# Kernel tuning notes

Hardware: AMD Instinct MI355X
Metric: run time of the kernel (lower is better)

Reference implementation:

```python
import jax, jax.numpy as jnp
import numpy as np

B, N, D = 32, 2048, 768
DEPTH, HEADS, GRID, NC = 12, 12, 10, 40
T = GRID * GRID + 1          # 100 pillars + cls token
HD = D // HEADS
SCALE = HD ** -0.5
INTERVAL = 0.2
MLP_H = 4 * D
EPS = 1e-5


def setup_inputs() -> dict:
    key = jax.random.key(0)
    ks = list(jax.random.split(key, 12))
    n = lambda k, s, std: (jax.random.normal(k, s, dtype=jnp.float32) * std)
    return {
        "x": jax.random.uniform(ks[0], (B, N, 3), minval=-1.0, maxval=1.0, dtype=jnp.float32),
        "W1": n(ks[1], (6, 32), 0.1),
        "W2": n(ks[2], (32, 64), 0.1),
        "W3": n(ks[3], (64, 128), 0.1),
        "Wa": n(ks[4], (256, D), 0.05),
        "bn_g": jnp.ones((GRID * GRID,), jnp.float32),
        "bn_b": jnp.zeros((GRID * GRID,), jnp.float32),
        "bn_mean": jnp.zeros((GRID * GRID,), jnp.float32),
        "bn_var": jnp.ones((GRID * GRID,), jnp.float32),
        "cls_token": jnp.zeros((1, 1, D), jnp.float32),
        "pos_embed": n(ks[5], (1, T, D), 0.02),
        "ln1_g": jnp.ones((DEPTH, D), jnp.float32), "ln1_b": jnp.zeros((DEPTH, D), jnp.float32),
        "qkv_w": n(ks[6], (DEPTH, D, 3 * D), 0.01),
        "proj_w": n(ks[7], (DEPTH, D, D), 0.01), "proj_b": jnp.zeros((DEPTH, D), jnp.float32),
        "ln2_g": jnp.ones((DEPTH, D), jnp.float32), "ln2_b": jnp.zeros((DEPTH, D), jnp.float32),
        "fc1_w": n(ks[8], (DEPTH, D, MLP_H), 0.01), "fc1_b": jnp.zeros((DEPTH, MLP_H), jnp.float32),
        "fc2_w": n(ks[9], (DEPTH, MLP_H, D), 0.01), "fc2_b": jnp.zeros((DEPTH, D), jnp.float32),
        "norm_g": jnp.ones((D,), jnp.float32), "norm_b": jnp.zeros((D,), jnp.float32),
        "head_w": n(ks[10], (D, NC), 0.01), "head_b": jnp.zeros((NC,), jnp.float32),
    }


def _layer_norm(x, g, b):
    m = jnp.mean(x, -1, keepdims=True)
    v = jnp.mean(jnp.square(x - m), -1, keepdims=True)
    return (x - m) * jax.lax.rsqrt(v + EPS) * g + b


def reference(x, W1, W2, W3, Wa, bn_g, bn_b, bn_mean, bn_var, cls_token, pos_embed,
              ln1_g, ln1_b, qkv_w, proj_w, proj_b, ln2_g, ln2_b,
              fc1_w, fc1_b, fc2_w, fc2_b, norm_g, norm_b, head_w, head_b):
    # ---- Pillar encoder (voxel bucketing via segment ops) ----
    # torch code reorders columns (y,z,x)->(z,y,x); voxel index uses (y,x)
    p = x[..., jnp.array([1, 0, 2])]                     # [B,N,3] = (z,y,x)
    yx = jnp.clip(p[..., 1:] + 1.0, 0.0, 1.99)
    idx = jnp.floor(yx / INTERVAL).astype(jnp.int32)     # [B,N,2] in [0,GRID)
    cell = (idx[..., 0] * GRID + idx[..., 1]
            + jnp.arange(B, dtype=jnp.int32)[:, None] * GRID * GRID).reshape(-1)
    pf = p.reshape(-1, 3)                                # [B*N,3]
    S = B * GRID * GRID
    cnt = jax.ops.segment_sum(jnp.ones((B * N,), pf.dtype), cell, num_segments=S)
    centroid = jax.ops.segment_sum(pf, cell, num_segments=S) / jnp.maximum(cnt, 1.0)[:, None]
    aug = jnp.concatenate([pf, pf - centroid[cell]], -1)  # [B*N,6]
    h = jax.nn.relu(aug @ W1)
    h = jax.nn.relu(h @ W2)
    h = jax.nn.relu(h @ W3)                               # [B*N,128]
    pooled = jax.ops.segment_max(h, cell, num_segments=S)  # per-pillar max
    h2 = jax.nn.relu(jnp.concatenate([h, pooled[cell]], -1) @ Wa)  # [B*N,768]
    pillar = jax.ops.segment_max(h2, cell, num_segments=S)
    pillar = jnp.where(cnt[:, None] > 0, pillar, 0.0)     # empty cells stay zero
    seq = pillar.reshape(B, GRID * GRID, D)               # flatten order = y*GRID+x
    # BatchNorm1d(100) over the sequence-position channel (eval mode)
    inv = bn_g * jax.lax.rsqrt(bn_var + EPS)
    seq = (seq - bn_mean[None, :, None]) * inv[None, :, None] + bn_b[None, :, None]

    # ---- ViT stack ----
    tokens = jnp.concatenate([jnp.broadcast_to(cls_token, (B, 1, D)), seq], 1) + pos_embed

    def block(hh, prm):
        g1, b1, qw, pw, pb, g2, b2, f1w, f1b, f2w, f2b = prm
        y = _layer_norm(hh, g1, b1)
        qkv = (y @ qw).reshape(B, T, 3, HEADS, HD)
        q, k, v = qkv[:, :, 0], qkv[:, :, 1], qkv[:, :, 2]   # [B,T,H,hd]
        attn = jax.nn.softmax(jnp.einsum('bqhd,bkhd->bhqk', q, k) * SCALE, -1)
        o = jnp.einsum('bhqk,bkhd->bqhd', attn, v).reshape(B, T, D)
        hh = hh + o @ pw + pb
        y = _layer_norm(hh, g2, b2)
        y = jax.nn.gelu(y @ f1w + f1b, approximate=False)
        hh = hh + y @ f2w + f2b
        return hh, None

    prms = (ln1_g, ln1_b, qkv_w, proj_w, proj_b, ln2_g, ln2_b, fc1_w, fc1_b, fc2_w, fc2_b)
    tokens, _ = jax.lax.scan(block, tokens, prms)
    out = _layer_norm(tokens, norm_g, norm_b)[:, 0] @ head_w + head_b  # cls head
    return out
```

## Files before the change

### kernel.cpp

```cpp
#include <hip/hip_runtime.h>

typedef __bf16 bf8 __attribute__((ext_vector_type(8)));
typedef float  f4  __attribute__((ext_vector_type(4)));
typedef unsigned long long uptr;

__device__ __forceinline__ void gload16(const void* g, void* l){
  __builtin_amdgcn_global_load_lds(
      (const __attribute__((address_space(1))) unsigned int*)(uptr)g,
      (__attribute__((address_space(3))) unsigned int*)(uptr)l,
      16, 0, 0);
}


__global__ __launch_bounds__(256) void k_cell(const float* __restrict__ x, int* __restrict__ cellArr,
                                              float* __restrict__ cnt, float* __restrict__ cent){
  int p = blockIdx.x*256 + threadIdx.x;
  float x0 = x[p*3+0], x1 = x[p*3+1], x2 = x[p*3+2];
  float y0 = fminf(fmaxf(x0 + 1.0f, 0.0f), 1.99f);
  float y1 = fminf(fmaxf(x2 + 1.0f, 0.0f), 1.99f);
  int i0 = (int)floorf(y0 / 0.2f);
  int i1 = (int)floorf(y1 / 0.2f);
  int b = p >> 11;
  int cell = b*100 + i0*10 + i1;
  cellArr[p] = cell;
  atomicAdd(&cnt[cell], 1.0f);
  atomicAdd(&cent[cell*3+0], x1);
  atomicAdd(&cent[cell*3+1], x0);
  atomicAdd(&cent[cell*3+2], x2);
}

__global__ void k_centdiv(float* cent, const float* cnt){
  int i = blockIdx.x*256 + threadIdx.x;
  if (i < 3200*3) cent[i] /= fmaxf(cnt[i/3], 1.0f);
}

__global__ __launch_bounds__(256) void k_scan(const float* __restrict__ cnt,
                                              int* __restrict__ base, int* __restrict__ wptr){
  __shared__ int a[256];
  int tid = threadIdx.x;
  int start = tid*13, end = start+13; if (end > 3200) end = 3200;
  int local = 0;
  for (int i = start; i < end; i++) local += (int)cnt[i];
  a[tid] = local;
  __syncthreads();
  for (int off = 1; off < 256; off <<= 1){
    int t = (tid >= off) ? a[tid - off] : 0;
    __syncthreads();
    a[tid] += t;
    __syncthreads();
  }
  int run = a[tid] - local;
  for (int i = start; i < end; i++){
    base[i] = run; wptr[i] = run;
    run += (int)cnt[i];
  }
}

__global__ __launch_bounds__(256) void k_scatter(const int* __restrict__ cellArr,
                                                 int* __restrict__ wptr, int* __restrict__ order){
  int p = blockIdx.x*256 + threadIdx.x;
  int c = cellArr[p];
  int pos = atomicAdd(&wptr[c], 1);
  order[pos] = p;
}

__global__ __launch_bounds__(256) void k_pointmlp(const float* __restrict__ x,
    const float* __restrict__ W1, const float* __restrict__ W2, const float* __restrict__ W3,
    const float* __restrict__ cent, const int* __restrict__ cellArr,
    const int* __restrict__ order, int* __restrict__ cellSlot, __bf16* __restrict__ A2){
  __shared__ float w1s[6*32];
  __shared__ float w2s[32*64];
  __shared__ float w3s[64*128];
  int tid = threadIdx.x;
  for (int i = tid; i < 192;  i += 256) w1s[i] = W1[i];
  for (int i = tid; i < 2048; i += 256) w2s[i] = W2[i];
  for (int i = tid; i < 8192; i += 256) w3s[i] = W3[i];
  __syncthreads();
  int s = blockIdx.x*256 + tid;
  int p = order[s];
  int cell = cellArr[p];
  cellSlot[s] = cell;
  float pf0 = x[p*3+1], pf1 = x[p*3+0], pf2 = x[p*3+2];
  float a[6] = {pf0, pf1, pf2, pf0 - cent[cell*3+0], pf1 - cent[cell*3+1], pf2 - cent[cell*3+2]};
  float h1[32];
  #pragma unroll
  for (int f = 0; f < 32; f++){
    float t = 0.f;
    #pragma unroll
    for (int i = 0; i < 6; i++) t += a[i]*w1s[i*32+f];
    h1[f] = fmaxf(t, 0.f);
  }
  float h2[64];
  #pragma unroll
  for (int f = 0; f < 64; f++){
    float t = 0.f;
    #pragma unroll
    for (int i = 0; i < 32; i++) t += h1[i]*w2s[i*64+f];
    h2[f] = fmaxf(t, 0.f);
  }
  for (int f0 = 0; f0 < 128; f0 += 8){
    __bf16 tmp[8];
    #pragma unroll
    for (int j = 0; j < 8; j++){
      float t = 0.f;
      #pragma unroll
      for (int i = 0; i < 64; i++) t += h2[i]*w3s[i*128+f0+j];
      tmp[j] = (__bf16)fmaxf(t, 0.f);
    }
    *reinterpret_cast<uint4*>(&A2[(size_t)s*256 + f0]) = *reinterpret_cast<uint4*>(tmp);
  }
}

__global__ __launch_bounds__(128) void k_poolh(const __bf16* __restrict__ A2,
    const int* __restrict__ base, const float* __restrict__ cnt, float* __restrict__ pooled){
  int c = blockIdx.x, f = threadIdx.x;
  int b0 = base[c], n = (int)cnt[c];
  float v = 0.f;
  for (int k = 0; k < n; k++) v = fmaxf(v, (float)A2[(size_t)(b0+k)*256 + f]);
  pooled[c*128 + f] = v;
}

__global__ __launch_bounds__(256) void k_fill(const float* __restrict__ pooled,
    const int* __restrict__ cellSlot, __bf16* __restrict__ A2){
  int idx = blockIdx.x*256 + threadIdx.x;
  int s = idx >> 7, f = idx & 127;
  A2[(size_t)s*256 + 128 + f] = (__bf16)pooled[cellSlot[s]*128 + f];
}

__global__ __launch_bounds__(256) void k_pillarpool(const __bf16* __restrict__ h2c,
    const int* __restrict__ base, const float* __restrict__ cnt, float* __restrict__ pillar, int cs){
  int c = blockIdx.x, tid = threadIdx.x;
  int b0 = base[c], e0 = b0 + (int)cnt[c];
  int lo = b0 > cs ? b0 : cs;
  int hi = e0 < cs + 16384 ? e0 : cs + 16384;
  if (lo >= hi) return;
  for (int f = tid; f < 768; f += 256){
    float v = 0.f;
    for (int s = lo; s < hi; s++) v = fmaxf(v, (float)h2c[(size_t)(s - cs)*768 + f]);
    atomicMax((int*)&pillar[(size_t)c*768 + f], __float_as_int(v));
  }
}

__global__ void k_assemble(const float* __restrict__ pillar,
    const float* __restrict__ bn_g, const float* __restrict__ bn_b,
    const float* __restrict__ bn_mean, const float* __restrict__ bn_var,
    const float* __restrict__ cls_t, const float* __restrict__ pos,
    float* __restrict__ tokens){
  int idx = blockIdx.x*256 + threadIdx.x;
  int m = idx / 768, d = idx % 768;
  int b = m / 101, t = m % 101;
  float v;
  if (t == 0) v = cls_t[d];
  else {
    int s = t - 1;
    float pv = pillar[((size_t)b*100 + s)*768 + d];
    float inv = bn_g[s]*rsqrtf(bn_var[s] + 1e-5f);
    v = (pv - bn_mean[s])*inv + bn_b[s];
  }
  tokens[idx] = v + pos[t*768 + d];
}


__global__ __launch_bounds__(256) void k_transpose(const float* __restrict__ W, __bf16* __restrict__ Wt,
                                                   int K, int N){
  __shared__ float t[32][33];
  int n0 = blockIdx.x*32, k0 = blockIdx.y*32;
  int tx = threadIdx.x & 31, ty = threadIdx.x >> 5;
  #pragma unroll
  for (int i = 0; i < 32; i += 8){
    int k = k0 + ty + i, n = n0 + tx;
    t[ty+i][tx] = (k < K && n < N) ? W[(size_t)k*N + n] : 0.f;
  }
  __syncthreads();
  #pragma unroll
  for (int i = 0; i < 32; i += 8){
    int n = n0 + ty + i, k = k0 + tx;
    if (n < N && k < K) Wt[(size_t)n*K + k] = (__bf16)t[tx][ty+i];
  }
}

__global__ __launch_bounds__(256) void k_transpose_all(
    const float* __restrict__ qw, const float* __restrict__ pw,
    const float* __restrict__ f1, const float* __restrict__ f2,
    __bf16* __restrict__ wq, __bf16* __restrict__ wp,
    __bf16* __restrict__ w1, __bf16* __restrict__ w2){
  int id = blockIdx.x;
  const float* W; __bf16* Wt; int K, N, nx, ny;
  if (id < 1728){ W=qw; Wt=wq; K=768;  N=2304; nx=id%72; ny=id/72; }
  else if (id < 2304){ id-=1728; W=pw; Wt=wp; K=768;  N=768;  nx=id%24; ny=id/24; }
  else if (id < 4608){ id-=2304; W=f1; Wt=w1; K=768;  N=3072; nx=id%96; ny=id/96; }
  else {               id-=4608; W=f2; Wt=w2; K=3072; N=768;  nx=id%24; ny=id/24; }
  __shared__ float t[32][33];
  int n0 = nx*32, k0 = ny*32;
  int tx = threadIdx.x & 31, ty = threadIdx.x >> 5;
  #pragma unroll
  for (int i = 0; i < 32; i += 8) t[ty+i][tx] = W[(size_t)(k0+ty+i)*N + n0+tx];
  __syncthreads();
  #pragma unroll
  for (int i = 0; i < 32; i += 8) Wt[(size_t)(n0+ty+i)*K + k0+tx] = (__bf16)t[tx][ty+i];
}


__global__ __launch_bounds__(256) void k_gemm(const __bf16* __restrict__ A, const __bf16* __restrict__ Bt,
    const float* __restrict__ bias, const float* __restrict__ res,
    float* __restrict__ outF, __bf16* __restrict__ outB,
    int M, int N, int K, int act, int splitK){
  __shared__ alignas(16) __bf16 As[128*32];
  __shared__ alignas(16) __bf16 Bs[128*32];
  int tid  = threadIdx.x;
  int m0 = blockIdx.y*128, n0 = blockIdx.x*128;
  int z = blockIdx.z;
  int kLen = K / splitK, k0 = z*kLen;
  int wave = tid >> 6, lane = tid & 63;
  int wm = (wave >> 1)*64, wn = (wave & 1)*64;
  int r16 = lane & 15, q = lane >> 4;
  int lrow = lane >> 2, lpc = lane & 3;
  f4 acc[4][4];
  #pragma unroll
  for (int i = 0; i < 4; i++)
    #pragma unroll
    for (int j = 0; j < 4; j++) acc[i][j] = (f4){0.f,0.f,0.f,0.f};

  for (int kt = k0; kt < k0 + kLen; kt += 32){
    #pragma unroll
    for (int s = 0; s < 2; s++){
      int rg  = wave*2 + s;
      int row = rg*16 + lrow;
      int gm = m0 + row; if (gm >= M) gm = M - 1;
      gload16(A  + (size_t)gm*K + kt + lpc*8, (char*)As + rg*1024 + lane*16);
      int gn = n0 + row;
      gload16(Bt + (size_t)gn*K + kt + lpc*8, (char*)Bs + rg*1024 + lane*16);
    }
    __syncthreads();
    bf8 af[4], bq[4];
    #pragma unroll
    for (int i = 0; i < 4; i++) af[i] = *reinterpret_cast<const bf8*>(&As[(wm + i*16 + r16)*32 + q*8]);
    #pragma unroll
    for (int j = 0; j < 4; j++) bq[j] = *reinterpret_cast<const bf8*>(&Bs[(wn + j*16 + r16)*32 + q*8]);
    #pragma unroll
    for (int i = 0; i < 4; i++)
      #pragma unroll
      for (int j = 0; j < 4; j++)
        acc[i][j] = __builtin_amdgcn_mfma_f32_16x16x32_bf16(af[i], bq[j], acc[i][j], 0, 0, 0);
    __syncthreads();
  }

  #pragma unroll
  for (int i = 0; i < 4; i++){
    #pragma unroll
    for (int j = 0; j < 4; j++){
      int nn = n0 + wn + j*16 + r16;
      float bv = (bias && z == 0) ? bias[nn] : 0.f;
      #pragma unroll
      for (int r = 0; r < 4; r++){
        int m = m0 + wm + i*16 + q*4 + r;
        if (m >= M) continue;
        float v = acc[i][j][r] + bv;
        if (splitK > 1){
          atomicAdd(&outF[(size_t)m*N + nn], v);
        } else {
          if (act == 1) v = fmaxf(v, 0.f);
          else if (act == 2) v = 0.5f*v*(1.f + erff(v*0.70710678118654752f));
          if (outB){
            outB[(size_t)m*N + nn] = (__bf16)v;
          } else {
            float rv = res ? res[(size_t)m*N + nn] : 0.f;
            outF[(size_t)m*N + nn] = rv + v;
          }
        }
      }
    }
  }
}


__global__ __launch_bounds__(256) void k_ln(const float* __restrict__ in, const float* __restrict__ g,
    const float* __restrict__ bta, __bf16* __restrict__ outB, float* __restrict__ outF, int rowMul){
  int orow = blockIdx.x;
  const float* xr = in + (size_t)orow*rowMul*768;
  int tid = threadIdx.x;
  float v0 = xr[tid], v1 = xr[tid+256], v2 = xr[tid+512];
  float s = v0+v1+v2, s2 = v0*v0 + v1*v1 + v2*v2;
  #pragma unroll
  for (int off = 32; off > 0; off >>= 1){ s += __shfl_xor(s, off); s2 += __shfl_xor(s2, off); }
  __shared__ float rs[4], rq[4];
  int w = tid >> 6;
  if ((tid & 63) == 0){ rs[w] = s; rq[w] = s2; }
  __syncthreads();
  s = rs[0]+rs[1]+rs[2]+rs[3]; s2 = rq[0]+rq[1]+rq[2]+rq[3];
  float mean = s*(1.f/768.f);
  float var  = s2*(1.f/768.f) - mean*mean;
  float rstd = rsqrtf(var + 1e-5f);
  size_t ob = (size_t)orow*768;
  float y0 = (v0-mean)*rstd*g[tid]     + bta[tid];
  float y1 = (v1-mean)*rstd*g[tid+256] + bta[tid+256];
  float y2 = (v2-mean)*rstd*g[tid+512] + bta[tid+512];
  if (outB){ outB[ob+tid]=(__bf16)y0; outB[ob+tid+256]=(__bf16)y1; outB[ob+tid+512]=(__bf16)y2; }
  else     { outF[ob+tid]=y0;         outF[ob+tid+256]=y1;         outF[ob+tid+512]=y2; }
}


#define PSS 136
#define VTS 136

__global__ __launch_bounds__(256) void k_attn(const __bf16* __restrict__ qkvB, __bf16* __restrict__ o){
  __shared__ alignas(16) __bf16 smem[64*VTS + 128*PSS];
  __bf16* Vt = smem;
  __bf16* Ps = smem + 64*VTS;
  int b = blockIdx.x / 12, h = blockIdx.x % 12;
  int tid = threadIdx.x;
  const __bf16* basep = qkvB + (size_t)(b*101)*2304 + h*64;

  #pragma unroll
  for (int it = 0; it < 4; it++){
    int c = tid + it*256;
    int t = c >> 3, d0 = c & 7;
    bf8 v;
    if (t < 101){
      v = *reinterpret_cast<const bf8*>(&basep[(size_t)t*2304 + 1536 + d0*8]);
    } else {
      #pragma unroll
      for (int j = 0; j < 8; j++) v[j] = (__bf16)0.f;
    }
    #pragma unroll
    for (int j = 0; j < 8; j++){
      int jj = (j + d0) & 7;
      Vt[(d0*8 + jj)*VTS + t] = v[jj];
    }
  }

  int wave = tid >> 6, lane = tid & 63;
  int r16 = lane & 15, q = lane >> 4;

  f4 sacc[2][7];
  #pragma unroll
  for (int rt = 0; rt < 2; rt++)
    #pragma unroll
    for (int j = 0; j < 7; j++) sacc[rt][j] = (f4){0.f,0.f,0.f,0.f};
  #pragma unroll
  for (int kt = 0; kt < 64; kt += 32){
    bf8 aq[2];
    #pragma unroll
    for (int rt = 0; rt < 2; rt++){
      int row = (wave + rt*4)*16 + r16; if (row > 100) row = 100;
      aq[rt] = *reinterpret_cast<const bf8*>(&basep[(size_t)row*2304 + kt + q*8]);
    }
    #pragma unroll
    for (int j = 0; j < 7; j++){
      int krow = j*16 + r16; if (krow > 100) krow = 100;
      bf8 kf = *reinterpret_cast<const bf8*>(&basep[(size_t)krow*2304 + 768 + kt + q*8]);
      #pragma unroll
      for (int rt = 0; rt < 2; rt++)
        sacc[rt][j] = __builtin_amdgcn_mfma_f32_16x16x32_bf16(aq[rt], kf, sacc[rt][j], 0, 0, 0);
    }
  }

  #pragma unroll
  for (int rt = 0; rt < 2; rt++){
    int m0 = (wave + rt*4)*16;
    #pragma unroll
    for (int r = 0; r < 4; r++){
      float s[7];
      #pragma unroll
      for (int j = 0; j < 7; j++){
        s[j] = sacc[rt][j][r] * 0.125f;
        if (j == 6 && r16 >= 5) s[j] = -1e30f;
      }
      float mx = s[0];
      #pragma unroll
      for (int j = 1; j < 7; j++) mx = fmaxf(mx, s[j]);
      #pragma unroll
      for (int off2 = 1; off2 < 16; off2 <<= 1) mx = fmaxf(mx, __shfl_xor(mx, off2));
      float p[7], sum = 0.f;
      #pragma unroll
      for (int j = 0; j < 7; j++){ p[j] = __expf(s[j] - mx); sum += p[j]; }
      #pragma unroll
      for (int off2 = 1; off2 < 16; off2 <<= 1) sum += __shfl_xor(sum, off2);
      float inv = 1.f / sum;
      int row = m0 + q*4 + r;
      #pragma unroll
      for (int j = 0; j < 7; j++) Ps[row*PSS + j*16 + r16] = (__bf16)(p[j]*inv);
      Ps[row*PSS + 112 + r16] = (__bf16)0.f;
    }
  }
  __syncthreads();

  f4 oacc[2][4];
  #pragma unroll
  for (int rt = 0; rt < 2; rt++)
    #pragma unroll
    for (int n = 0; n < 4; n++) oacc[rt][n] = (f4){0.f,0.f,0.f,0.f};
  #pragma unroll
  for (int kt = 0; kt < 128; kt += 32){
    bf8 af[2];
    #pragma unroll
    for (int rt = 0; rt < 2; rt++)
      af[rt] = *reinterpret_cast<const bf8*>(&Ps[((wave + rt*4)*16 + r16)*PSS + kt + q*8]);
    #pragma unroll
    for (int n = 0; n < 4; n++){
      bf8 bq = *reinterpret_cast<const bf8*>(&Vt[(n*16 + r16)*VTS + kt + q*8]);
      #pragma unroll
      for (int rt = 0; rt < 2; rt++)
        oacc[rt][n] = __builtin_amdgcn_mfma_f32_16x16x32_bf16(af[rt], bq, oacc[rt][n], 0, 0, 0);
    }
  }

  #pragma unroll
  for (int rt = 0; rt < 2; rt++){
    int m0 = (wave + rt*4)*16;
    #pragma unroll
    for (int n = 0; n < 4; n++){
      #pragma unroll
      for (int r = 0; r < 4; r++){
        int t = m0 + q*4 + r;
        if (t < 101)
          o[((size_t)(b*101 + t))*768 + h*64 + n*16 + r16] = (__bf16)oacc[rt][n][r];
      }
    }
  }
}

__global__ void k_head(const float* __restrict__ cls, const float* __restrict__ hw,
                       const float* __restrict__ hb, float* __restrict__ out){
  int b = blockIdx.x, c = threadIdx.x;
  if (c < 40){
    float s = hb[c];
    for (int k = 0; k < 768; k++) s += cls[b*768 + k]*hw[k*40 + c];
    out[b*40 + c] = s;
  }
}


extern "C" void kernel_launch(void* const* d_in, const int* in_sizes, int n_in,
                              void* d_out, int out_size, void* d_ws, size_t ws_size,
                              hipStream_t stream){
  const float* x       = (const float*)d_in[0];
  const float* W1      = (const float*)d_in[1];
  const float* W2      = (const float*)d_in[2];
  const float* W3      = (const float*)d_in[3];
  const float* Wa      = (const float*)d_in[4];
  const float* bn_g    = (const float*)d_in[5];
  const float* bn_b    = (const float*)d_in[6];
  const float* bn_mean = (const float*)d_in[7];
  const float* bn_var  = (const float*)d_in[8];
  const float* cls_t   = (const float*)d_in[9];
  const float* pos     = (const float*)d_in[10];
  const float* ln1_g   = (const float*)d_in[11];
  const float* ln1_b   = (const float*)d_in[12];
  const float* qkv_w   = (const float*)d_in[13];
  const float* proj_w  = (const float*)d_in[14];
  const float* proj_b  = (const float*)d_in[15];
  const float* ln2_g   = (const float*)d_in[16];
  const float* ln2_b   = (const float*)d_in[17];
  const float* fc1_w   = (const float*)d_in[18];
  const float* fc1_b   = (const float*)d_in[19];
  const float* fc2_w   = (const float*)d_in[20];
  const float* fc2_b   = (const float*)d_in[21];
  const float* norm_g  = (const float*)d_in[22];
  const float* norm_b  = (const float*)d_in[23];
  const float* head_w  = (const float*)d_in[24];
  const float* head_b  = (const float*)d_in[25];

  char* ws = (char*)d_ws;
  size_t off = 0;
  auto alloc = [&](size_t bytes)->void*{ void* p = ws + off; off += (bytes + 255) & ~(size_t)255; return p; };
  float* cnt     = (float*)alloc(3200*4);
  float* cent    = (float*)alloc(3200*3*4);
  float* pillar  = (float*)alloc((size_t)3200*768*4);
  size_t zbytes  = (size_t)((char*)pillar - (char*)cnt) + (size_t)3200*768*4;
  int*   base    = (int*)  alloc(3200*4);
  int*   wptr    = (int*)  alloc(3200*4);
  int*   order   = (int*)  alloc((size_t)65536*4);
  int*   cellSlot= (int*)  alloc((size_t)65536*4);
  int*   cellArr = (int*)  alloc((size_t)65536*4);
  float* pooled  = (float*)alloc((size_t)3200*128*4);
  float* tokens  = (float*)alloc((size_t)3232*768*4);
  float* cls     = (float*)alloc((size_t)32*768*4);
  __bf16* wWa    = (__bf16*)alloc((size_t)768*256*2);
  size_t offR = off;
  __bf16* A2  = (__bf16*)alloc((size_t)65536*256*2);
  __bf16* h2c = (__bf16*)alloc((size_t)16384*768*2);
  size_t endPillarPhase = off;
  off = offR;
  __bf16* y    = (__bf16*)alloc((size_t)3232*768*2);
  __bf16* qkvB = (__bf16*)alloc((size_t)3232*2304*2);
  __bf16* o    = (__bf16*)alloc((size_t)3232*768*2);
  __bf16* mlp  = (__bf16*)alloc((size_t)3232*3072*2);
  __bf16* wq   = (__bf16*)alloc((size_t)768*2304*2);
  __bf16* wp   = (__bf16*)alloc((size_t)768*768*2);
  __bf16* w1   = (__bf16*)alloc((size_t)768*3072*2);
  __bf16* w2   = (__bf16*)alloc((size_t)3072*768*2);
  if (off < endPillarPhase) off = endPillarPhase;
  (void)ws_size; (void)in_sizes; (void)n_in; (void)out_size;

  hipMemsetAsync(cnt, 0, zbytes, stream);

  k_cell<<<256,256,0,stream>>>(x, cellArr, cnt, cent);
  k_centdiv<<<38,256,0,stream>>>(cent, cnt);
  k_scan<<<1,256,0,stream>>>(cnt, base, wptr);
  k_scatter<<<256,256,0,stream>>>(cellArr, wptr, order);
  k_pointmlp<<<256,256,0,stream>>>(x, W1, W2, W3, cent, cellArr, order, cellSlot, A2);
  k_poolh<<<3200,128,0,stream>>>(A2, base, cnt, pooled);
  k_fill<<<32768,256,0,stream>>>(pooled, cellSlot, A2);
  k_transpose<<<dim3(24,8),256,0,stream>>>(Wa, wWa, 256, 768);
  for (int c = 0; c < 4; c++){
    k_gemm<<<dim3(6,128),256,0,stream>>>(A2 + (size_t)c*16384*256, wWa, nullptr, nullptr,
                                         nullptr, h2c, 16384, 768, 256, 1, 1);
    k_pillarpool<<<3200,256,0,stream>>>(h2c, base, cnt, pillar, c*16384);
  }
  k_assemble<<<9696,256,0,stream>>>(pillar, bn_g, bn_b, bn_mean, bn_var, cls_t, pos, tokens);

  for (int l = 0; l < 12; l++){
    k_transpose_all<<<6912,256,0,stream>>>(qkv_w + (size_t)l*768*2304, proj_w + (size_t)l*768*768,
                                           fc1_w + (size_t)l*768*3072, fc2_w + (size_t)l*3072*768,
                                           wq, wp, w1, w2);
    k_ln<<<3232,256,0,stream>>>(tokens, ln1_g + l*768, ln1_b + l*768, y, nullptr, 1);
    k_gemm<<<dim3(18,26),256,0,stream>>>(y, wq, nullptr, nullptr, nullptr, qkvB, 3232, 2304, 768, 0, 1);
    k_attn<<<384,256,0,stream>>>(qkvB, o);
    k_gemm<<<dim3(6,26,4),256,0,stream>>>(o, wp, proj_b + l*768, nullptr, tokens, nullptr,
                                          3232, 768, 768, 0, 4);
    k_ln<<<3232,256,0,stream>>>(tokens, ln2_g + l*768, ln2_b + l*768, y, nullptr, 1);
    k_gemm<<<dim3(24,26),256,0,stream>>>(y, w1, fc1_b + l*3072, nullptr, nullptr, mlp, 3232, 3072, 768, 2, 1);
    k_gemm<<<dim3(6,26,4),256,0,stream>>>(mlp, w2, fc2_b + l*768, nullptr, tokens, nullptr,
                                          3232, 768, 3072, 0, 4);
  }

  k_ln<<<32,256,0,stream>>>(tokens, norm_g, norm_b, nullptr, cls, 101);
  k_head<<<32,64,0,stream>>>(cls, head_w, head_b, (float*)d_out);
}
```

Measured before the change: 3.131 ms.

## Batch weight transposes, deepen GEMM K-tile with swizzle, split attention blocks

All 12 layers' weights are transposed to bf16 in one up-front launch instead of per layer, using extra workspace. The GEMM K-tile grows from 32 to 64 with an XOR-swizzled LDS layout to halve barrier count and avoid bank conflicts. Attention is split into two blocks per (batch, head) with a smaller LDS footprint and a launch-bounds occupancy hint. The centroid divide is folded into the point MLP, and the fill kernel now writes 16-byte vectors.

New measurement: 2.906 ms. 7.2% less time.

```diff
diff --git a/kernel.cpp b/kernel.cpp
--- a/kernel.cpp
+++ b/kernel.cpp
@@ -29,11 +29,6 @@
   atomicAdd(&cent[cell*3+2], x2);
 }
 
-__global__ void k_centdiv(float* cent, const float* cnt){
-  int i = blockIdx.x*256 + threadIdx.x;
-  if (i < 3200*3) cent[i] /= fmaxf(cnt[i/3], 1.0f);
-}
-
 __global__ __launch_bounds__(256) void k_scan(const float* __restrict__ cnt,
                                               int* __restrict__ base, int* __restrict__ wptr){
   __shared__ int a[256];
@@ -66,7 +61,7 @@
 
 __global__ __launch_bounds__(256) void k_pointmlp(const float* __restrict__ x,
     const float* __restrict__ W1, const float* __restrict__ W2, const float* __restrict__ W3,
-    const float* __restrict__ cent, const int* __restrict__ cellArr,
+    const float* __restrict__ cent, const float* __restrict__ cnt, const int* __restrict__ cellArr,
     const int* __restrict__ order, int* __restrict__ cellSlot, __bf16* __restrict__ A2){
   __shared__ float w1s[6*32];
   __shared__ float w2s[32*64];
@@ -81,7 +76,9 @@
   int cell = cellArr[p];
   cellSlot[s] = cell;
   float pf0 = x[p*3+1], pf1 = x[p*3+0], pf2 = x[p*3+2];
-  float a[6] = {pf0, pf1, pf2, pf0 - cent[cell*3+0], pf1 - cent[cell*3+1], pf2 - cent[cell*3+2]};
+  float cc = fmaxf(cnt[cell], 1.0f);
+  float a[6] = {pf0, pf1, pf2,
+                pf0 - cent[cell*3+0]/cc, pf1 - cent[cell*3+1]/cc, pf2 - cent[cell*3+2]/cc};
   float h1[32];
   #pragma unroll
   for (int f = 0; f < 32; f++){
@@ -123,8 +120,13 @@
 __global__ __launch_bounds__(256) void k_fill(const float* __restrict__ pooled,
     const int* __restrict__ cellSlot, __bf16* __restrict__ A2){
   int idx = blockIdx.x*256 + threadIdx.x;
-  int s = idx >> 7, f = idx & 127;
-  A2[(size_t)s*256 + 128 + f] = (__bf16)pooled[cellSlot[s]*128 + f];
+  int s = idx >> 4, f0 = (idx & 15) << 3;
+  int cell = cellSlot[s];
+  const float* pp = &pooled[cell*128 + f0];
+  __bf16 tmp[8];
+  #pragma unroll
+  for (int j = 0; j < 8; j++) tmp[j] = (__bf16)pp[j];
+  *reinterpret_cast<uint4*>(&A2[(size_t)s*256 + 128 + f0]) = *reinterpret_cast<uint4*>(tmp);
 }
 
 __global__ __launch_bounds__(256) void k_pillarpool(const __bf16* __restrict__ h2c,
@@ -185,11 +187,12 @@
     __bf16* __restrict__ wq, __bf16* __restrict__ wp,
     __bf16* __restrict__ w1, __bf16* __restrict__ w2){
   int id = blockIdx.x;
+  size_t l = blockIdx.y;
   const float* W; __bf16* Wt; int K, N, nx, ny;
-  if (id < 1728){ W=qw; Wt=wq; K=768;  N=2304; nx=id%72; ny=id/72; }
-  else if (id < 2304){ id-=1728; W=pw; Wt=wp; K=768;  N=768;  nx=id%24; ny=id/24; }
-  else if (id < 4608){ id-=2304; W=f1; Wt=w1; K=768;  N=3072; nx=id%96; ny=id/96; }
-  else {               id-=4608; W=f2; Wt=w2; K=3072; N=768;  nx=id%24; ny=id/24; }
+  if (id < 1728){ W=qw+l*768*2304; Wt=wq+l*768*2304; K=768;  N=2304; nx=id%72; ny=id/72; }
+  else if (id < 2304){ id-=1728; W=pw+l*768*768;  Wt=wp+l*768*768;  K=768;  N=768;  nx=id%24; ny=id/24; }
+  else if (id < 4608){ id-=2304; W=f1+l*768*3072; Wt=w1+l*768*3072; K=768;  N=3072; nx=id%96; ny=id/96; }
+  else {               id-=4608; W=f2+l*3072*768; Wt=w2+l*3072*768; K=3072; N=768;  nx=id%24; ny=id/24; }
   __shared__ float t[32][33];
   int n0 = nx*32, k0 = ny*32;
   int tx = threadIdx.x & 31, ty = threadIdx.x >> 5;
@@ -205,8 +208,8 @@
     const float* __restrict__ bias, const float* __restrict__ res,
     float* __restrict__ outF, __bf16* __restrict__ outB,
     int M, int N, int K, int act, int splitK){
-  __shared__ alignas(16) __bf16 As[128*32];
-  __shared__ alignas(16) __bf16 Bs[128*32];
+  __shared__ alignas(16) __bf16 As[128*64];
+  __shared__ alignas(16) __bf16 Bs[128*64];
   int tid  = threadIdx.x;
   int m0 = blockIdx.y*128, n0 = blockIdx.x*128;
   int z = blockIdx.z;
@@ -214,34 +217,41 @@
   int wave = tid >> 6, lane = tid & 63;
   int wm = (wave >> 1)*64, wn = (wave & 1)*64;
   int r16 = lane & 15, q = lane >> 4;
-  int lrow = lane >> 2, lpc = lane & 3;
+  int srow = tid >> 3;
+  int sslot = tid & 7;
+  int slotX[2];
+  #pragma unroll
+  for (int kk = 0; kk < 2; kk++) slotX[kk] = ((kk*4 + q) ^ (r16 & 7)) * 8;
   f4 acc[4][4];
   #pragma unroll
   for (int i = 0; i < 4; i++)
     #pragma unroll
     for (int j = 0; j < 4; j++) acc[i][j] = (f4){0.f,0.f,0.f,0.f};
 
-  for (int kt = k0; kt < k0 + kLen; kt += 32){
-    #pragma unroll
-    for (int s = 0; s < 2; s++){
-      int rg  = wave*2 + s;
-      int row = rg*16 + lrow;
+  for (int kt = k0; kt < k0 + kLen; kt += 64){
+    #pragma unroll
+    for (int rr = 0; rr < 4; rr++){
+      int row = rr*32 + srow;
+      int scol = kt + ((sslot ^ (row & 7)) * 8);
       int gm = m0 + row; if (gm >= M) gm = M - 1;
-      gload16(A  + (size_t)gm*K + kt + lpc*8, (char*)As + rg*1024 + lane*16);
+      gload16(A  + (size_t)gm*K + scol, (char*)As + rr*4096 + tid*16);
       int gn = n0 + row;
-      gload16(Bt + (size_t)gn*K + kt + lpc*8, (char*)Bs + rg*1024 + lane*16);
+      gload16(Bt + (size_t)gn*K + scol, (char*)Bs + rr*4096 + tid*16);
     }
     __syncthreads();
-    bf8 af[4], bq[4];
-    #pragma unroll
-    for (int i = 0; i < 4; i++) af[i] = *reinterpret_cast<const bf8*>(&As[(wm + i*16 + r16)*32 + q*8]);
-    #pragma unroll
-    for (int j = 0; j < 4; j++) bq[j] = *reinterpret_cast<const bf8*>(&Bs[(wn + j*16 + r16)*32 + q*8]);
-    #pragma unroll
-    for (int i = 0; i < 4; i++)
+    #pragma unroll
+    for (int kk = 0; kk < 2; kk++){
+      bf8 af[4], bq[4];
       #pragma unroll
-      for (int j = 0; j < 4; j++)
-        acc[i][j] = __builtin_amdgcn_mfma_f32_16x16x32_bf16(af[i], bq[j], acc[i][j], 0, 0, 0);
+      for (int i = 0; i < 4; i++) af[i] = *reinterpret_cast<const bf8*>(&As[(wm + i*16 + r16)*64 + slotX[kk]]);
+      #pragma unroll
+      for (int j = 0; j < 4; j++) bq[j] = *reinterpret_cast<const bf8*>(&Bs[(wn + j*16 + r16)*64 + slotX[kk]]);
+      #pragma unroll
+      for (int i = 0; i < 4; i++)
+        #pragma unroll
+        for (int j = 0; j < 4; j++)
+          acc[i][j] = __builtin_amdgcn_mfma_f32_16x16x32_bf16(af[i], bq[j], acc[i][j], 0, 0, 0);
+    }
     __syncthreads();
   }
 
@@ -303,11 +313,12 @@
 #define PSS 136
 #define VTS 136
 
-__global__ __launch_bounds__(256) void k_attn(const __bf16* __restrict__ qkvB, __bf16* __restrict__ o){
-  __shared__ alignas(16) __bf16 smem[64*VTS + 128*PSS];
+__global__ __launch_bounds__(256, 3) void k_attn(const __bf16* __restrict__ qkvB, __bf16* __restrict__ o){
+  __shared__ alignas(16) __bf16 smem[64*VTS + 64*PSS];
   __bf16* Vt = smem;
   __bf16* Ps = smem + 64*VTS;
-  int b = blockIdx.x / 12, h = blockIdx.x % 12;
+  int bh = blockIdx.x >> 1, half = blockIdx.x & 1;
+  int b = bh / 12, h = bh % 12;
   int tid = threadIdx.x;
   const __bf16* basep = qkvB + (size_t)(b*101)*2304 + h*64;
 
@@ -331,91 +342,69 @@
 
   int wave = tid >> 6, lane = tid & 63;
   int r16 = lane & 15, q = lane >> 4;
-
-  f4 sacc[2][7];
-  #pragma unroll
-  for (int rt = 0; rt < 2; rt++)
-    #pragma unroll
-    for (int j = 0; j < 7; j++) sacc[rt][j] = (f4){0.f,0.f,0.f,0.f};
+  int m0 = half*64 + wave*16;
+
+  f4 sacc[7];
+  #pragma unroll
+  for (int j = 0; j < 7; j++) sacc[j] = (f4){0.f,0.f,0.f,0.f};
   #pragma unroll
   for (int kt = 0; kt < 64; kt += 32){
-    bf8 aq[2];
-    #pragma unroll
-    for (int rt = 0; rt < 2; rt++){
-      int row = (wave + rt*4)*16 + r16; if (row > 100) row = 100;
-      aq[rt] = *reinterpret_cast<const bf8*>(&basep[(size_t)row*2304 + kt + q*8]);
-    }
+    int row = m0 + r16; if (row > 100) row = 100;
+    bf8 aq = *reinterpret_cast<const bf8*>(&basep[(size_t)row*2304 + kt + q*8]);
     #pragma unroll
     for (int j = 0; j < 7; j++){
       int krow = j*16 + r16; if (krow > 100) krow = 100;
       bf8 kf = *reinterpret_cast<const bf8*>(&basep[(size_t)krow*2304 + 768 + kt + q*8]);
-      #pragma unroll
-      for (int rt = 0; rt < 2; rt++)
-        sacc[rt][j] = __builtin_amdgcn_mfma_f32_16x16x32_bf16(aq[rt], kf, sacc[rt][j], 0, 0, 0);
-    }
-  }
-
-  #pragma unroll
-  for (int rt = 0; rt < 2; rt++){
-    int m0 = (wave + rt*4)*16;
-    #pragma unroll
-    for (int r = 0; r < 4; r++){
-      float s[7];
-      #pragma unroll
-      for (int j = 0; j < 7; j++){
-        s[j] = sacc[rt][j][r] * 0.125f;
-        if (j == 6 && r16 >= 5) s[j] = -1e30f;
-      }
-      float mx = s[0];
-      #pragma unroll
-      for (int j = 1; j < 7; j++) mx = fmaxf(mx, s[j]);
-      #pragma unroll
-      for (int off2 = 1; off2 < 16; off2 <<= 1) mx = fmaxf(mx, __shfl_xor(mx, off2));
-      float p[7], sum = 0.f;
-      #pragma unroll
-      for (int j = 0; j < 7; j++){ p[j] = __expf(s[j] - mx); sum += p[j]; }
-      #pragma unroll
-      for (int off2 = 1; off2 < 16; off2 <<= 1) sum += __shfl_xor(sum, off2);
-      float inv = 1.f / sum;
-      int row = m0 + q*4 + r;
-      #pragma unroll
-      for (int j = 0; j < 7; j++) Ps[row*PSS + j*16 + r16] = (__bf16)(p[j]*inv);
-      Ps[row*PSS + 112 + r16] = (__bf16)0.f;
-    }
+      sacc[j] = __builtin_amdgcn_mfma_f32_16x16x32_bf16(aq, kf, sacc[j], 0, 0, 0);
+    }
+  }
+
+  #pragma unroll
+  for (int r = 0; r < 4; r++){
+    float s[7];
+    #pragma unroll
+    for (int j = 0; j < 7; j++){
+      s[j] = sacc[j][r] * 0.125f;
+      if (j == 6 && r16 >= 5) s[j] = -1e30f;
+    }
+    float mx = s[0];
+    #pragma unroll
+    for (int j = 1; j < 7; j++) mx = fmaxf(mx, s[j]);
+    #pragma unroll
+    for (int off2 = 1; off2 < 16; off2 <<= 1) mx = fmaxf(mx, __shfl_xor(mx, off2));
+    float p[7], sum = 0.f;
+    #pragma unroll
+    for (int j = 0; j < 7; j++){ p[j] = __expf(s[j] - mx); sum += p[j]; }
+    #pragma unroll
+    for (int off2 = 1; off2 < 16; off2 <<= 1) sum += __shfl_xor(sum, off2);
+    float inv = 1.f / sum;
+    int lr = wave*16 + q*4 + r;
+    #pragma unroll
+    for (int j = 0; j < 7; j++) Ps[lr*PSS + j*16 + r16] = (__bf16)(p[j]*inv);
+    Ps[lr*PSS + 112 + r16] = (__bf16)0.f;
   }
   __syncthreads();
 
-  f4 oacc[2][4];
-  #pragma unroll
-  for (int rt = 0; rt < 2; rt++)
-    #pragma unroll
-    for (int n = 0; n < 4; n++) oacc[rt][n] = (f4){0.f,0.f,0.f,0.f};
+  f4 oacc[4];
+  #pragma unroll
+  for (int n = 0; n < 4; n++) oacc[n] = (f4){0.f,0.f,0.f,0.f};
   #pragma unroll
   for (int kt = 0; kt < 128; kt += 32){
-    bf8 af[2];
-    #pragma unroll
-    for (int rt = 0; rt < 2; rt++)
-      af[rt] = *reinterpret_cast<const bf8*>(&Ps[((wave + rt*4)*16 + r16)*PSS + kt + q*8]);
+    bf8 af = *reinterpret_cast<const bf8*>(&Ps[(wave*16 + r16)*PSS + kt + q*8]);
     #pragma unroll
     for (int n = 0; n < 4; n++){
       bf8 bq = *reinterpret_cast<const bf8*>(&Vt[(n*16 + r16)*VTS + kt + q*8]);
-      #pragma unroll
-      for (int rt = 0; rt < 2; rt++)
-        oacc[rt][n] = __builtin_amdgcn_mfma_f32_16x16x32_bf16(af[rt], bq, oacc[rt][n], 0, 0, 0);
-    }
-  }
-
-  #pragma unroll
-  for (int rt = 0; rt < 2; rt++){
-    int m0 = (wave + rt*4)*16;
-    #pragma unroll
-    for (int n = 0; n < 4; n++){
-      #pragma unroll
-      for (int r = 0; r < 4; r++){
-        int t = m0 + q*4 + r;
-        if (t < 101)
-          o[((size_t)(b*101 + t))*768 + h*64 + n*16 + r16] = (__bf16)oacc[rt][n][r];
-      }
+      oacc[n] = __builtin_amdgcn_mfma_f32_16x16x32_bf16(af, bq, oacc[n], 0, 0, 0);
+    }
+  }
+
+  #pragma unroll
+  for (int n = 0; n < 4; n++){
+    #pragma unroll
+    for (int r = 0; r < 4; r++){
+      int t = m0 + q*4 + r;
+      if (t < 101)
+        o[((size_t)(b*101 + t))*768 + h*64 + n*16 + r16] = (__bf16)oacc[n][r];
     }
   }
 }
@@ -477,6 +466,10 @@
   float* tokens  = (float*)alloc((size_t)3232*768*4);
   float* cls     = (float*)alloc((size_t)32*768*4);
   __bf16* wWa    = (__bf16*)alloc((size_t)768*256*2);
+  __bf16* wq12   = (__bf16*)alloc((size_t)12*768*2304*2);
+  __bf16* wp12   = (__bf16*)alloc((size_t)12*768*768*2);
+  __bf16* w112   = (__bf16*)alloc((size_t)12*768*3072*2);
+  __bf16* w212   = (__bf16*)alloc((size_t)12*3072*768*2);
   size_t offR = off;
   __bf16* A2  = (__bf16*)alloc((size_t)65536*256*2);
   __bf16* h2c = (__bf16*)alloc((size_t)16384*768*2);
@@ -486,23 +479,20 @@
   __bf16* qkvB = (__bf16*)alloc((size_t)3232*2304*2);
   __bf16* o    = (__bf16*)alloc((size_t)3232*768*2);
   __bf16* mlp  = (__bf16*)alloc((size_t)3232*3072*2);
-  __bf16* wq   = (__bf16*)alloc((size_t)768*2304*2);
-  __bf16* wp   = (__bf16*)alloc((size_t)768*768*2);
-  __bf16* w1   = (__bf16*)alloc((size_t)768*3072*2);
-  __bf16* w2   = (__bf16*)alloc((size_t)3072*768*2);
   if (off < endPillarPhase) off = endPillarPhase;
   (void)ws_size; (void)in_sizes; (void)n_in; (void)out_size;
 
   hipMemsetAsync(cnt, 0, zbytes, stream);
 
+  k_transpose_all<<<dim3(6912,12),256,0,stream>>>(qkv_w, proj_w, fc1_w, fc2_w, wq12, wp12, w112, w212);
+  k_transpose<<<dim3(24,8),256,0,stream>>>(Wa, wWa, 256, 768);
+
   k_cell<<<256,256,0,stream>>>(x, cellArr, cnt, cent);
-  k_centdiv<<<38,256,0,stream>>>(cent, cnt);
   k_scan<<<1,256,0,stream>>>(cnt, base, wptr);
   k_scatter<<<256,256,0,stream>>>(cellArr, wptr, order);
-  k_pointmlp<<<256,256,0,stream>>>(x, W1, W2, W3, cent, cellArr, order, cellSlot, A2);
+  k_pointmlp<<<256,256,0,stream>>>(x, W1, W2, W3, cent, cnt, cellArr, order, cellSlot, A2);
   k_poolh<<<3200,128,0,stream>>>(A2, base, cnt, pooled);
-  k_fill<<<32768,256,0,stream>>>(pooled, cellSlot, A2);
-  k_transpose<<<dim3(24,8),256,0,stream>>>(Wa, wWa, 256, 768);
+  k_fill<<<4096,256,0,stream>>>(pooled, cellSlot, A2);
   for (int c = 0; c < 4; c++){
     k_gemm<<<dim3(6,128),256,0,stream>>>(A2 + (size_t)c*16384*256, wWa, nullptr, nullptr,
                                          nullptr, h2c, 16384, 768, 256, 1, 1);
@@ -511,12 +501,13 @@
   k_assemble<<<9696,256,0,stream>>>(pillar, bn_g, bn_b, bn_mean, bn_var, cls_t, pos, tokens);
 
   for (int l = 0; l < 12; l++){
-    k_transpose_all<<<6912,256,0,stream>>>(qkv_w + (size_t)l*768*2304, proj_w + (size_t)l*768*768,
-                                           fc1_w + (size_t)l*768*3072, fc2_w + (size_t)l*3072*768,
-                                           wq, wp, w1, w2);
+    __bf16* wq = wq12 + (size_t)l*768*2304;
+    __bf16* wp = wp12 + (size_t)l*768*768;
+    __bf16* w1 = w112 + (size_t)l*768*3072;
+    __bf16* w2 = w212 + (size_t)l*3072*768;
     k_ln<<<3232,256,0,stream>>>(tokens, ln1_g + l*768, ln1_b + l*768, y, nullptr, 1);
     k_gemm<<<dim3(18,26),256,0,stream>>>(y, wq, nullptr, nullptr, nullptr, qkvB, 3232, 2304, 768, 0, 1);
-    k_attn<<<384,256,0,stream>>>(qkvB, o);
+    k_attn<<<768,256,0,stream>>>(qkvB, o);
     k_gemm<<<dim3(6,26,4),256,0,stream>>>(o, wp, proj_b + l*768, nullptr, tokens, nullptr,
                                           3232, 768, 768, 0, 4);
     k_ln<<<3232,256,0,stream>>>(tokens, ln2_g + l*768, ln2_b + l*768, y, nullptr, 1);
```
